# Kernel tuning notes

Measured on AMD Instinct MI355X. Metric: run time of the kernel, lower is better.

The kernel has to match this reference:

```python
import jax, jax.numpy as jnp
import numpy as np


def cheb_mats(N: int, degree: int):
    """Analysis/synthesis Chebyshev matrices, matching torch reference.
    Returns T_pinv [d+1, N], T_eval [N, d+1] as float32 jnp arrays."""
    x = np.linspace(0.0, 1.0, N, dtype=np.float32)
    xn = np.clip(2.0 * x - 1.0, -1 + 1e-06, 1 - 1e-06)
    theta = np.arccos(xn)
    ks = np.arange(degree + 1, dtype=np.float32)
    T = np.cos(theta[:, None] * ks[None, :])  # [N, d+1]
    T_pinv = np.linalg.pinv(T.astype(np.float64)).astype(np.float32)  # [d+1, N]
    return jnp.asarray(T_pinv), jnp.asarray(T.astype(np.float32))


def setup_inputs() -> dict:
    key = jax.random.key(0)
    k1, k2, k3 = jax.random.split(key, 3)
    B, C, H, W = 32, 64, 128, 128
    out_ch, degree = 64, 8
    scale_w = (2.0 / (C * (degree + 1))) ** 0.5
    scale_h = (2.0 / (out_ch * (degree + 1))) ** 0.5
    x = jax.random.normal(k1, (B, C, H, W), dtype=jnp.float32)
    W_w = scale_w * jax.random.normal(k2, (C, out_ch, degree + 1), dtype=jnp.float32)
    W_h = scale_h * jax.random.normal(k3, (out_ch, out_ch, degree + 1), dtype=jnp.float32)
    return {"x": x, "W_w": W_w, "W_h": W_h}


def reference(x, W_w, W_h):
    B, C, H, W = x.shape
    degree = W_w.shape[-1] - 1
    Tp_w, Te_w = cheb_mats(W, degree)  # [k,W], [W,k]
    Tp_h, Te_h = cheb_mats(H, degree)  # [k,H], [H,k]
    # --- mix along width axis with W_w (equivalent to torch's B*H batched 1D) ---
    c = jnp.einsum('bchw,kw->bchk', x, Tp_w)      # analysis: coeffs over width
    m = jnp.einsum('bchk,cok->bohk', c, W_w)      # channel mixing per degree
    y = jnp.einsum('bohk,wk->bohw', m, Te_w)      # synthesis back to width grid
    # --- mix along height axis with W_h ---
    c2 = jnp.einsum('bohw,kh->bokw', y, Tp_h)
    m2 = jnp.einsum('bokw,ofk->bfkw', c2, W_h)
    out = jnp.einsum('bfkw,hk->bfhw', m2, Te_h)   # [B, out_ch, H, W]
    return out
```

## Files before the change

kernel.cpp:

```cpp
#include <hip/hip_runtime.h>
#include <math.h>


#define K9 9

__global__ __launch_bounds__(256) void setup_all(const float* __restrict__ Ww,
                                                 const float* __restrict__ Wh,
                                                 float* __restrict__ Tp,
                                                 float* __restrict__ Te,
                                                 float* __restrict__ Tpt16,
                                                 float* __restrict__ Wt_w,
                                                 float* __restrict__ Wh_f,
                                                 float* __restrict__ d_ws) {
    int tid = threadIdx.x;
    if (blockIdx.x != 0) {
        int gid = (blockIdx.x - 1) * 256 + tid;
        if (gid < 36864) {
            int k = gid / 4096, r = gid % 4096, c = r / 64, o = r % 64;
            Wt_w[gid] = Ww[(c * 64 + o) * 9 + k];
        } else if (gid < 73728) {
            int g = gid - 36864;
            int f = g / 576, r = g % 576, kh = r / 64, o = r % 64;
            Wh_f[g] = Wh[(o * 64 + f) * 9 + kh];
        } else if (gid < 115200) {
            int g = gid - 73728;
            ((float4*)d_ws)[g] = make_float4(0.f, 0.f, 0.f, 0.f);
        }
        return;
    }
    __shared__ double Tsh[128 * K9];
    __shared__ double GA[9][18];
    if (tid < 128) {
        int n = tid;
        float xf = (float)((double)n / 127.0);
        float xn = 2.0f * xf - 1.0f;
        const float lo = (float)(-1.0 + 1e-6);
        const float hi = (float)(1.0 - 1e-6);
        xn = fminf(fmaxf(xn, lo), hi);
        float th = acosf(xn);
        for (int k = 0; k < K9; ++k) {
            float tv = cosf(th * (float)k);
            Te[n * K9 + k] = tv;
            Tsh[n * K9 + k] = (double)tv;
        }
    }
    __syncthreads();
    if (tid < 81) {
        int i = tid / 9, j = tid % 9;
        double s = 0.0;
        for (int n = 0; n < 128; ++n) s += Tsh[n * K9 + i] * Tsh[n * K9 + j];
        GA[i][j] = s;
    }
    if (tid >= 81 && tid < 162) {
        int i = (tid - 81) / 9, j = (tid - 81) % 9;
        GA[i][9 + j] = (i == j) ? 1.0 : 0.0;
    }
    __syncthreads();
    int r18 = tid / 18, j18 = tid % 18;
    for (int col = 0; col < 9; ++col) {
        double inv = 0.0;
        if (tid < 18) inv = 1.0 / GA[col][col];
        __syncthreads();
        if (tid < 18) GA[col][tid] *= inv;
        __syncthreads();
        double f = 0.0;
        if (tid < 162 && r18 != col) f = GA[r18][col];
        __syncthreads();
        if (tid < 162 && r18 != col) GA[r18][j18] -= f * GA[col][j18];
        __syncthreads();
    }
    for (int idx = tid; idx < K9 * 128; idx += 256) {
        int k = idx / 128, n = idx % 128;
        double s = 0.0;
        for (int j = 0; j < 9; ++j) s += GA[k][9 + j] * Tsh[n * K9 + j];
        float sv = (float)s;
        Tp[idx] = sv;
        Tpt16[n * 16 + k] = sv;
    }
}

__global__ __launch_bounds__(256, 2) void k1_width(const float* __restrict__ x,
                                                   const float* __restrict__ Wt_w,
                                                   const float* __restrict__ Tpt16,
                                                   const float* __restrict__ Tp,
                                                   float* __restrict__ d_ws) {
    __shared__ float xs_red[2 * 64 * 129];
    __shared__ float cs[4 * 64 * K9];
    float* xs = xs_red;
    float* red = xs_red;
    int tid = threadIdx.x;
    int b  = blockIdx.x >> 5;
    int h0 = (blockIdx.x & 31) << 2;
    int c   = tid & 63;
    int wid = tid >> 6;
    int hh2 = wid >> 1;
    int q   = wid & 1;
    int qu  = __builtin_amdgcn_readfirstlane(q);
    const float* tpq = Tpt16 + qu * 64 * 16;
    const float* xb = x + (size_t)b * 1048576;

    for (int ch = 0; ch < 2; ++ch) {
        __syncthreads();
        for (int it = 0; it < 16; ++it) {
            int e = it * 256 + tid;
            int hh2s = e >> 11;
            int e2 = e & 2047;
            int cc = e2 >> 5;
            int w4 = (e2 & 31) << 2;
            float4 v = *(const float4*)(xb + (size_t)cc * 16384 +
                                        (size_t)(h0 + ch * 2 + hh2s) * 128 + w4);
            float* dst = &xs[hh2s * 8256 + cc * 129 + w4];
            dst[0] = v.x; dst[1] = v.y; dst[2] = v.z; dst[3] = v.w;
        }
        __syncthreads();
        float acc[K9];
#pragma unroll
        for (int k = 0; k < K9; ++k) acc[k] = 0.f;
        const float* xr = &xs[hh2 * 8256 + c * 129 + qu * 64];
#pragma unroll 8
        for (int w6 = 0; w6 < 64; ++w6) {
            float xv = xr[w6];
            const float* tr = tpq + w6 * 16;
#pragma unroll
            for (int k = 0; k < K9; ++k) acc[k] = fmaf(xv, tr[k], acc[k]);
        }
        __syncthreads();
        float* rw = &red[(wid * 64 + c) * K9];
#pragma unroll
        for (int k = 0; k < K9; ++k) rw[k] = acc[k];
        __syncthreads();
        for (int idx = tid; idx < 2 * 64 * K9; idx += 256) {
            int hh2r = idx / 576, rem = idx - hh2r * 576;
            float v0 = red[(2 * hh2r) * 576 + rem];
            float v1 = red[(2 * hh2r + 1) * 576 + rem];
            cs[(ch * 2 + hh2r) * 576 + rem] = v0 + v1;
        }
    }
    __syncthreads();
    float* db = d_ws + (size_t)b * 5184;
    const float* tph = Tp + h0;
    for (int idx = tid; idx < 576; idx += 256) {
        int o = idx & 63, k = idx >> 6;
        const float* wt = Wt_w + k * 4096 + o;
        float a0 = 0.f, a1 = 0.f, a2 = 0.f, a3 = 0.f;
        for (int cc = 0; cc < 64; ++cc) {
            float wv = wt[cc * 64];
            float i0 = cs[0 * 576 + cc * 9 + k];
            float i1 = cs[1 * 576 + cc * 9 + k];
            float i2 = cs[2 * 576 + cc * 9 + k];
            float i3 = cs[3 * 576 + cc * 9 + k];
            a0 = fmaf(i0, wv, a0); a1 = fmaf(i1, wv, a1);
            a2 = fmaf(i2, wv, a2); a3 = fmaf(i3, wv, a3);
        }
#pragma unroll
        for (int kh = 0; kh < K9; ++kh) {
            float t0 = tph[kh * 128 + 0];
            float t1 = tph[kh * 128 + 1];
            float t2 = tph[kh * 128 + 2];
            float t3 = tph[kh * 128 + 3];
            float contrib = fmaf(a0, t0, fmaf(a1, t1, fmaf(a2, t2, a3 * t3)));
            atomicAdd(db + kh * 576 + idx, contrib);
        }
    }
}

__global__ __launch_bounds__(256) void k3_synth(const float* __restrict__ d_ws,
                                                const float* __restrict__ Wh_f,
                                                const float* __restrict__ Te,
                                                float* __restrict__ out) {
    __shared__ float ds[81 * 65];
    __shared__ float whs[9 * 65];
    __shared__ float tes[1152];
    __shared__ float f1[9 * 128];
    __shared__ float el[81];
    int tid = threadIdx.x;
    int bf = blockIdx.x;
    int b = bf >> 6, f = bf & 63;
    const float* db = d_ws + (size_t)b * 5184;
    for (int i = tid; i < 5184; i += 256) ds[(i >> 6) * 65 + (i & 63)] = db[i];
    const float* whf = Wh_f + (size_t)f * 576;
    for (int i = tid; i < 576; i += 256) whs[(i >> 6) * 65 + (i & 63)] = whf[i];
    for (int i = tid; i < 1152; i += 256) tes[i] = Te[i];
    __syncthreads();
    if (tid < 81) {
        int kh = tid / 9;
        const float* wr = &whs[kh * 65];
        const float* dr = &ds[tid * 65];
        float ea = 0.f;
#pragma unroll 8
        for (int o = 0; o < 64; ++o) ea = fmaf(wr[o], dr[o], ea);
        el[tid] = ea;
    }
    __syncthreads();
    for (int idx = tid; idx < 1152; idx += 256) {
        int kh = idx >> 7, w = idx & 127;
        float acc = 0.f;
#pragma unroll
        for (int kw = 0; kw < 9; ++kw)
            acc = fmaf(el[kh * 9 + kw], tes[w * 9 + kw], acc);
        f1[kh * 128 + w] = acc;
    }
    __syncthreads();
    int w4 = (tid & 31) << 2;
    int hg = tid >> 5;
    float4 fr[9];
#pragma unroll
    for (int k = 0; k < 9; ++k) fr[k] = *(const float4*)&f1[k * 128 + w4];
    float* ob = out + (size_t)bf * 16384;
    for (int h = hg; h < 128; h += 8) {
        const float* th = &tes[h * 9];
        float4 acc = make_float4(0.f, 0.f, 0.f, 0.f);
#pragma unroll
        for (int k = 0; k < 9; ++k) {
            float t = th[k];
            acc.x = fmaf(t, fr[k].x, acc.x);
            acc.y = fmaf(t, fr[k].y, acc.y);
            acc.z = fmaf(t, fr[k].z, acc.z);
            acc.w = fmaf(t, fr[k].w, acc.w);
        }
        *(float4*)(ob + h * 128 + w4) = acc;
    }
}

extern "C" void kernel_launch(void* const* d_in, const int* in_sizes, int n_in,
                              void* d_out, int out_size, void* d_ws, size_t ws_size,
                              hipStream_t stream) {
    (void)in_sizes; (void)n_in; (void)out_size; (void)ws_size;
    const float* x  = (const float*)d_in[0];
    const float* Ww = (const float*)d_in[1];
    const float* Wh = (const float*)d_in[2];
    float* out = (float*)d_out;
    float* ws = (float*)d_ws;
    float* Tp    = ws;
    float* Te    = ws + 1152;
    float* Tpt16 = ws + 2304;
    float* Wt_w  = ws + 4352;
    float* Wh_f  = ws + 41216;
    float* d_d   = ws + 78080;

    setup_all<<<451, 256, 0, stream>>>(Ww, Wh, Tp, Te, Tpt16, Wt_w, Wh_f, d_d);
    k1_width<<<1024, 256, 0, stream>>>(x, Wt_w, Tpt16, Tp, d_d);
    k3_synth<<<2048, 256, 0, stream>>>(d_d, Wh_f, Te, out);
}
```

Baseline: 299.7 us.

## Process eight rows per block with register prefetch and four-way width split in k1

The width-analysis kernel now handles 8 height rows per block (512 blocks instead of 1024). Each row's x slice is prefetched into registers while the current row is computed, and each wave covers a quarter of the width with float4 shared-memory reads. Channel mixing then amortizes each weight load over 8 rows and issues half as many atomics in total. The synth kernel's global-to-shared loads are switched to float4. The intended gain is better latency hiding and fewer atomics, at the cost of higher register pressure and fewer blocks to spread across the GPU.

```diff
diff --git a/kernel.cpp b/kernel.cpp
--- a/kernel.cpp
+++ b/kernel.cpp
@@ -84,82 +84,96 @@
                                                    const float* __restrict__ Tpt16,
                                                    const float* __restrict__ Tp,
                                                    float* __restrict__ d_ws) {
-    __shared__ float xs_red[2 * 64 * 129];
-    __shared__ float cs[4 * 64 * K9];
-    float* xs = xs_red;
-    float* red = xs_red;
+    __shared__ float xs[64 * 132];
+    __shared__ float red[4 * 64 * K9];
+    __shared__ float cs[64 * 76];
     int tid = threadIdx.x;
-    int b  = blockIdx.x >> 5;
-    int h0 = (blockIdx.x & 31) << 2;
+    int b  = blockIdx.x >> 4;
+    int h0 = (blockIdx.x & 15) << 3;
     int c   = tid & 63;
     int wid = tid >> 6;
-    int hh2 = wid >> 1;
-    int q   = wid & 1;
-    int qu  = __builtin_amdgcn_readfirstlane(q);
-    const float* tpq = Tpt16 + qu * 64 * 16;
+    int qu  = __builtin_amdgcn_readfirstlane(wid);
+    const float* tpq = Tpt16 + qu * 512;
     const float* xb = x + (size_t)b * 1048576;
 
-    for (int ch = 0; ch < 2; ++ch) {
-        __syncthreads();
-        for (int it = 0; it < 16; ++it) {
-            int e = it * 256 + tid;
-            int hh2s = e >> 11;
-            int e2 = e & 2047;
-            int cc = e2 >> 5;
-            int w4 = (e2 & 31) << 2;
-            float4 v = *(const float4*)(xb + (size_t)cc * 16384 +
-                                        (size_t)(h0 + ch * 2 + hh2s) * 128 + w4);
-            float* dst = &xs[hh2s * 8256 + cc * 129 + w4];
-            dst[0] = v.x; dst[1] = v.y; dst[2] = v.z; dst[3] = v.w;
-        }
-        __syncthreads();
+#pragma unroll
+    for (int it = 0; it < 8; ++it) {
+        int e = it * 256 + tid;
+        int cc = e >> 5, w4 = (e & 31) << 2;
+        *(float4*)&xs[cc * 132 + w4] =
+            *(const float4*)(xb + (size_t)cc * 16384 + (size_t)h0 * 128 + w4);
+    }
+    __syncthreads();
+
+    float4 pf[8];
+    for (int r = 0; r < 8; ++r) {
+        if (r < 7) {
+#pragma unroll
+            for (int it = 0; it < 8; ++it) {
+                int e = it * 256 + tid;
+                int cc = e >> 5, w4 = (e & 31) << 2;
+                pf[it] = *(const float4*)(xb + (size_t)cc * 16384 +
+                                          (size_t)(h0 + r + 1) * 128 + w4);
+            }
+        }
         float acc[K9];
 #pragma unroll
         for (int k = 0; k < K9; ++k) acc[k] = 0.f;
-        const float* xr = &xs[hh2 * 8256 + c * 129 + qu * 64];
-#pragma unroll 8
-        for (int w6 = 0; w6 < 64; ++w6) {
-            float xv = xr[w6];
-            const float* tr = tpq + w6 * 16;
-#pragma unroll
-            for (int k = 0; k < K9; ++k) acc[k] = fmaf(xv, tr[k], acc[k]);
-        }
-        __syncthreads();
+        const float* xr = &xs[c * 132 + qu * 32];
+#pragma unroll
+        for (int w6 = 0; w6 < 8; ++w6) {
+            float4 xv = *(const float4*)&xr[w6 * 4];
+            const float* tr = tpq + w6 * 64;
+#pragma unroll
+            for (int k = 0; k < K9; ++k) {
+                acc[k] = fmaf(xv.x, tr[k],      acc[k]);
+                acc[k] = fmaf(xv.y, tr[16 + k], acc[k]);
+                acc[k] = fmaf(xv.z, tr[32 + k], acc[k]);
+                acc[k] = fmaf(xv.w, tr[48 + k], acc[k]);
+            }
+        }
         float* rw = &red[(wid * 64 + c) * K9];
 #pragma unroll
         for (int k = 0; k < K9; ++k) rw[k] = acc[k];
         __syncthreads();
-        for (int idx = tid; idx < 2 * 64 * K9; idx += 256) {
-            int hh2r = idx / 576, rem = idx - hh2r * 576;
-            float v0 = red[(2 * hh2r) * 576 + rem];
-            float v1 = red[(2 * hh2r + 1) * 576 + rem];
-            cs[(ch * 2 + hh2r) * 576 + rem] = v0 + v1;
-        }
-    }
-    __syncthreads();
+        for (int idx = tid; idx < 576; idx += 256) {
+            float v = red[idx] + red[576 + idx] + red[1152 + idx] + red[1728 + idx];
+            int cc2 = idx / 9, kk = idx - cc2 * 9;
+            cs[cc2 * 76 + kk * 8 + r] = v;
+        }
+        if (r < 7) {
+#pragma unroll
+            for (int it = 0; it < 8; ++it) {
+                int e = it * 256 + tid;
+                int cc = e >> 5, w4 = (e & 31) << 2;
+                *(float4*)&xs[cc * 132 + w4] = pf[it];
+            }
+        }
+        __syncthreads();
+    }
+
     float* db = d_ws + (size_t)b * 5184;
     const float* tph = Tp + h0;
     for (int idx = tid; idx < 576; idx += 256) {
         int o = idx & 63, k = idx >> 6;
         const float* wt = Wt_w + k * 4096 + o;
         float a0 = 0.f, a1 = 0.f, a2 = 0.f, a3 = 0.f;
+        float a4 = 0.f, a5 = 0.f, a6 = 0.f, a7 = 0.f;
         for (int cc = 0; cc < 64; ++cc) {
             float wv = wt[cc * 64];
-            float i0 = cs[0 * 576 + cc * 9 + k];
-            float i1 = cs[1 * 576 + cc * 9 + k];
-            float i2 = cs[2 * 576 + cc * 9 + k];
-            float i3 = cs[3 * 576 + cc * 9 + k];
-            a0 = fmaf(i0, wv, a0); a1 = fmaf(i1, wv, a1);
-            a2 = fmaf(i2, wv, a2); a3 = fmaf(i3, wv, a3);
+            float4 p0 = *(const float4*)&cs[cc * 76 + k * 8];
+            float4 p1 = *(const float4*)&cs[cc * 76 + k * 8 + 4];
+            a0 = fmaf(p0.x, wv, a0); a1 = fmaf(p0.y, wv, a1);
+            a2 = fmaf(p0.z, wv, a2); a3 = fmaf(p0.w, wv, a3);
+            a4 = fmaf(p1.x, wv, a4); a5 = fmaf(p1.y, wv, a5);
+            a6 = fmaf(p1.z, wv, a6); a7 = fmaf(p1.w, wv, a7);
         }
 #pragma unroll
         for (int kh = 0; kh < K9; ++kh) {
-            float t0 = tph[kh * 128 + 0];
-            float t1 = tph[kh * 128 + 1];
-            float t2 = tph[kh * 128 + 2];
-            float t3 = tph[kh * 128 + 3];
-            float contrib = fmaf(a0, t0, fmaf(a1, t1, fmaf(a2, t2, a3 * t3)));
-            atomicAdd(db + kh * 576 + idx, contrib);
+            const float* t = tph + kh * 128;
+            float ctr = fmaf(a0, t[0], fmaf(a1, t[1], fmaf(a2, t[2], a3 * t[3])));
+            ctr = fmaf(a4, t[4], fmaf(a5, t[5], fmaf(a6, t[6], fmaf(a7, t[7], ctr))));
+            atomicAdd(db + kh * 576 + idx, ctr);
         }
     }
 }
@@ -176,11 +190,19 @@
     int tid = threadIdx.x;
     int bf = blockIdx.x;
     int b = bf >> 6, f = bf & 63;
-    const float* db = d_ws + (size_t)b * 5184;
-    for (int i = tid; i < 5184; i += 256) ds[(i >> 6) * 65 + (i & 63)] = db[i];
-    const float* whf = Wh_f + (size_t)f * 576;
-    for (int i = tid; i < 576; i += 256) whs[(i >> 6) * 65 + (i & 63)] = whf[i];
-    for (int i = tid; i < 1152; i += 256) tes[i] = Te[i];
+    const float4* db4 = (const float4*)(d_ws + (size_t)b * 5184);
+    for (int i = tid; i < 1296; i += 256) {
+        float4 v = db4[i];
+        float* dst = &ds[(i >> 4) * 65 + ((i & 15) << 2)];
+        dst[0] = v.x; dst[1] = v.y; dst[2] = v.z; dst[3] = v.w;
+    }
+    const float4* wh4 = (const float4*)(Wh_f + (size_t)f * 576);
+    for (int i = tid; i < 144; i += 256) {
+        float4 v = wh4[i];
+        float* dst = &whs[(i >> 4) * 65 + ((i & 15) << 2)];
+        dst[0] = v.x; dst[1] = v.y; dst[2] = v.z; dst[3] = v.w;
+    }
+    for (int i = tid; i < 288; i += 256) ((float4*)tes)[i] = ((const float4*)Te)[i];
     __syncthreads();
     if (tid < 81) {
         int kh = tid / 9;
@@ -239,6 +261,6 @@
     float* d_d   = ws + 78080;
 
     setup_all<<<451, 256, 0, stream>>>(Ww, Wh, Tp, Te, Tpt16, Wt_w, Wh_f, d_d);
-    k1_width<<<1024, 256, 0, stream>>>(x, Wt_w, Tpt16, Tp, d_d);
+    k1_width<<<512, 256, 0, stream>>>(x, Wt_w, Tpt16, Tp, d_d);
     k3_synth<<<2048, 256, 0, stream>>>(d_d, Wh_f, Te, out);
 }
```

New measurement: 389.8 us. 30.1% more time.
